# Kernel tuning notes

Measured on AMD Instinct MI355X. Metric: run time of the kernel, lower is better.

The kernel has to match this reference:

```python
import jax, jax.numpy as jnp
import numpy as np

B, T, D, H = 8, 512, 1024, 16
DH = D // H  # per-head feature dim (64)


def setup_inputs() -> dict:
    key = jax.random.key(0)
    ks = jax.random.split(key, 10)
    s = 1.0 / np.sqrt(DH)
    inp = {
        "X_data": jax.random.normal(ks[0], (B, T, D), dtype=jnp.float32),
        "mask": jnp.ones((B, T), dtype=jnp.int32),
        # per-head Q/K/V projections (each SelfAttention has its own d_h x d_h weights)
        "Wq": jax.random.normal(ks[1], (H, DH, DH), dtype=jnp.float32) * s,
        "bq": jnp.zeros((H, DH), dtype=jnp.float32),
        "Wk": jax.random.normal(ks[2], (H, DH, DH), dtype=jnp.float32) * s,
        "bk": jnp.zeros((H, DH), dtype=jnp.float32),
        "Wv": jax.random.normal(ks[3], (H, DH, DH), dtype=jnp.float32) * s,
        "bv": jnp.zeros((H, DH), dtype=jnp.float32),
        # AttentionFusion: linear on concatenated head outputs -> len_feature_new
        "Wf": jax.random.normal(ks[4], (D, D), dtype=jnp.float32) * (1.0 / np.sqrt(D)),
        "bf": jnp.zeros((D,), dtype=jnp.float32),
    }
    return inp


def reference(X_data, mask, Wq, bq, Wk, bk, Wv, bv, Wf, bf):
    # Split features into heads: [B, T, H, DH] (equal partitions since D % H == 0)
    Xh = X_data.reshape(B, T, H, DH)
    # Batched per-head projections (replaces the Python loop over heads)
    Q = jnp.einsum("bthd,hde->bhte", Xh, Wq) + bq[None, :, None, :]
    K = jnp.einsum("bthd,hde->bhte", Xh, Wk) + bk[None, :, None, :]
    V = jnp.einsum("bthd,hde->bhte", Xh, Wv) + bv[None, :, None, :]
    scale = 1.0 / jnp.sqrt(jnp.asarray(DH, dtype=Q.dtype))
    scores = jnp.einsum("bhqe,bhke->bhqk", Q, K) * scale  # [B, H, T, T]
    scores = jnp.where(mask[:, None, None, :] > 0, scores, jnp.asarray(-1e9, scores.dtype))
    att = jax.nn.softmax(scores, axis=-1)
    out = jnp.einsum("bhqk,bhke->bhqe", att, V)  # [B, H, T, DH]
    # Concatenate heads (same order as the per-head loop) and fuse
    out = out.transpose(0, 2, 1, 3).reshape(B, T, D)
    fused = out @ Wf + bf  # AttentionFusion linear
    return fused
```

## Files before the change

kernel.cpp:

```cpp
#include <hip/hip_runtime.h>
#include <math.h>

#define B 8
#define T 512
#define D 1024
#define H 16
#define DH 64

typedef __bf16 bf16;
typedef __attribute__((ext_vector_type(8))) __bf16 bf16x8;
typedef __attribute__((ext_vector_type(4))) __bf16 bf16x4;
typedef __attribute__((ext_vector_type(4))) float f32x4;

__device__ __forceinline__ void gld16(const void* g, void* l) {
    __builtin_amdgcn_global_load_lds(
        (const __attribute__((address_space(1))) void*)g,
        (__attribute__((address_space(3))) void*)l, 16, 0, 0);
}


#define EXP2SCALE 1.44269504088896f

__global__ __launch_bounds__(256, 2) void qkv_attn(
    const float* __restrict__ X, const int* __restrict__ mask,
    const float* __restrict__ Wq, const float* __restrict__ Wk,
    const float* __restrict__ Wv,
    const float* __restrict__ bq, const float* __restrict__ bv,
    const float* __restrict__ Wf, bf16* __restrict__ WfT,
    bf16* __restrict__ Ob)
{
    __shared__ __align__(16) char smem[80384];

    if (blockIdx.x >= 512) {
        bf16* Ts = (bf16*)smem;
        const int ti = blockIdx.x - 512, tid = threadIdx.x;
        const int k0 = (ti >> 4) * 64, n0 = (ti & 15) * 64;
        for (int i = tid; i < 1024; i += 256) {
            const int k = i >> 4, nq = (i & 15) * 4;
            const float4 w = *(const float4*)(Wf + (size_t)(k0 + k) * D + n0 + nq);
            Ts[(nq + 0) * 72 + k] = (bf16)w.x; Ts[(nq + 1) * 72 + k] = (bf16)w.y;
            Ts[(nq + 2) * 72 + k] = (bf16)w.z; Ts[(nq + 3) * 72 + k] = (bf16)w.w;
        }
        __syncthreads();
        for (int i = tid; i < 512; i += 256) {
            const int n = i >> 3, kc = (i & 7) * 8;
            *(bf16x8*)(WfT + (size_t)(n0 + n) * D + k0 + kc) = *(const bf16x8*)&Ts[n * 72 + kc];
        }
        return;
    }

    bf16* Wks = (bf16*)(smem);
    bf16* Wvs = (bf16*)(smem + 8192);
    bf16* Pl  = (bf16*)(smem + 53248);
    bf16* Xkt = (bf16*)(smem + 71680);
    int*  msk = (int*)(smem + 79872);
    bf16* Wqs   = (bf16*)(smem + 16384);
    bf16* Xq    = Pl;
    bf16* Stage = Pl;
    bf16* Ostage = Pl;

    const int bh = blockIdx.x & 127, q0 = (blockIdx.x >> 7) * 128;
    const int b = bh >> 4, h = bh & 15;
    const int tid = threadIdx.x, wave = tid >> 6, lane = tid & 63;
    const int quad = lane >> 4, l15 = lane & 15;

    const int pkrow = wave * 16 + (lane >> 2);
    const int pc0 = (lane & 3) * 2;

    float bqr[4], bvr[4];
#pragma unroll
    for (int nt = 0; nt < 4; ++nt) {
        bqr[nt] = bq[h * DH + nt * 16 + l15];
        bvr[nt] = bv[h * DH + nt * 16 + l15];
    }

    float4 px0, px1, px2, px3;
    {
        const float* src = X + (size_t)(b * T + pkrow) * D + h * DH + pc0 * 8;
        px0 = *(const float4*)src; px1 = *(const float4*)(src + 4);
        px2 = *(const float4*)(src + 8); px3 = *(const float4*)(src + 12);
    }
    int mreg = (tid < 64) ? mask[(size_t)b * T + tid] : 0;

    for (int i = tid; i < 1024; i += 256) {
        const int d = i >> 4, eq4 = (i & 15) * 4;
        const float4 wq4 = *(const float4*)(Wq + (size_t)h * 4096 + d * 64 + eq4);
        const float4 wk4 = *(const float4*)(Wk + (size_t)h * 4096 + d * 64 + eq4);
        const float4 wv4 = *(const float4*)(Wv + (size_t)h * 4096 + d * 64 + eq4);
#pragma unroll
        for (int j = 0; j < 4; ++j) {
            const int e = eq4 + j;
            const int idx = e * 64 + (((d >> 3) ^ (e & 7)) * 8) + (d & 7);
            Wqs[idx] = (bf16)((const float*)&wq4)[j];
            Wks[idx] = (bf16)((const float*)&wk4)[j];
            Wvs[idx] = (bf16)((const float*)&wv4)[j];
        }
    }
    for (int i = tid; i < 1024; i += 256) {
        const int row = i >> 3, c = i & 7;
        const float* src = X + (size_t)(b * T + q0 + row) * D + h * DH + c * 8;
        const float4 x0 = *(const float4*)src;
        const float4 x1 = *(const float4*)(src + 4);
        bf16x8 t;
        t[0] = (bf16)x0.x; t[1] = (bf16)x0.y; t[2] = (bf16)x0.z; t[3] = (bf16)x0.w;
        t[4] = (bf16)x1.x; t[5] = (bf16)x1.y; t[6] = (bf16)x1.z; t[7] = (bf16)x1.w;
        *(bf16x8*)&Xq[row * 64 + ((c ^ (row & 7)) * 8)] = t;
    }
    __syncthreads();

    {
        f32x4 accQ[2][4] = {};
#pragma unroll
        for (int ks = 0; ks < 2; ++ks) {
            bf16x8 af[2], bfr[4];
#pragma unroll
            for (int mt = 0; mt < 2; ++mt) {
                const int row = wave * 32 + mt * 16 + l15;
                af[mt] = *(const bf16x8*)&Xq[row * 64 + (((ks * 4 + quad) ^ (l15 & 7)) * 8)];
            }
#pragma unroll
            for (int nt = 0; nt < 4; ++nt)
                bfr[nt] = *(const bf16x8*)&Wqs[(nt * 16 + l15) * 64 + (((ks * 4 + quad) ^ (l15 & 7)) * 8)];
#pragma unroll
            for (int mt = 0; mt < 2; ++mt)
#pragma unroll
                for (int nt = 0; nt < 4; ++nt)
                    accQ[mt][nt] = __builtin_amdgcn_mfma_f32_16x16x32_bf16(af[mt], bfr[nt], accQ[mt][nt], 0, 0, 0);
        }
        __syncthreads();
        const float qs = 0.125f * EXP2SCALE;
#pragma unroll
        for (int mt = 0; mt < 2; ++mt)
#pragma unroll
            for (int nt = 0; nt < 4; ++nt)
#pragma unroll
                for (int reg = 0; reg < 4; ++reg)
                    Stage[(wave * 32 + mt * 16 + quad * 4 + reg) * 72 + nt * 16 + l15] =
                        (bf16)((accQ[mt][nt][reg] + bqr[nt]) * qs);
        __builtin_amdgcn_wave_barrier();
    }
    bf16x8 qf[2][2];
#pragma unroll
    for (int mt = 0; mt < 2; ++mt)
#pragma unroll
        for (int ks = 0; ks < 2; ++ks)
            qf[mt][ks] = *(const bf16x8*)&Stage[(wave * 32 + mt * 16 + l15) * 72 + ks * 32 + quad * 8];

    f32x4 acc[2][4] = {};
    float lst2[2] = {0.f, 0.f};

    for (int kt = 0; kt < 8; ++kt) {
        const int p = kt & 1;
        bf16* Ks  = (bf16*)(smem + 16384 + p * 9216);
        bf16* Vts = (bf16*)(smem + 34816 + p * 9216);

        {
            bf16x8 t0, t1;
            t0[0] = (bf16)px0.x; t0[1] = (bf16)px0.y; t0[2] = (bf16)px0.z; t0[3] = (bf16)px0.w;
            t0[4] = (bf16)px1.x; t0[5] = (bf16)px1.y; t0[6] = (bf16)px1.z; t0[7] = (bf16)px1.w;
            t1[0] = (bf16)px2.x; t1[1] = (bf16)px2.y; t1[2] = (bf16)px2.z; t1[3] = (bf16)px2.w;
            t1[4] = (bf16)px3.x; t1[5] = (bf16)px3.y; t1[6] = (bf16)px3.z; t1[7] = (bf16)px3.w;
            *(bf16x8*)&Xkt[pkrow * 64 + ((pc0 ^ (pkrow & 7)) * 8)] = t0;
            *(bf16x8*)&Xkt[pkrow * 64 + (((pc0 + 1) ^ (pkrow & 7)) * 8)] = t1;
            if (tid < 64) msk[p * 64 + tid] = mreg;
        }
        __builtin_amdgcn_wave_barrier();

        if (kt < 7) {
            const float* src = X + (size_t)(b * T + (kt + 1) * 64 + pkrow) * D + h * DH + pc0 * 8;
            px0 = *(const float4*)src; px1 = *(const float4*)(src + 4);
            px2 = *(const float4*)(src + 8); px3 = *(const float4*)(src + 12);
            if (tid < 64) mreg = mask[(size_t)b * T + (kt + 1) * 64 + tid];
        }

        {
            bf16x8 afkv[2];
#pragma unroll
            for (int ks = 0; ks < 2; ++ks)
                afkv[ks] = *(const bf16x8*)&Xkt[(wave * 16 + l15) * 64 + (((ks * 4 + quad) ^ (l15 & 7)) * 8)];
            f32x4 accK[4] = {}, accV[4] = {};
            __builtin_amdgcn_s_setprio(1);
#pragma unroll
            for (int ks = 0; ks < 2; ++ks)
#pragma unroll
                for (int nt = 0; nt < 4; ++nt) {
                    const bf16x8 bk8 = *(const bf16x8*)&Wks[(nt * 16 + l15) * 64 + (((ks * 4 + quad) ^ (l15 & 7)) * 8)];
                    accK[nt] = __builtin_amdgcn_mfma_f32_16x16x32_bf16(bk8, afkv[ks], accK[nt], 0, 0, 0);
                    const bf16x8 bv8 = *(const bf16x8*)&Wvs[(nt * 16 + l15) * 64 + (((ks * 4 + quad) ^ (l15 & 7)) * 8)];
                    accV[nt] = __builtin_amdgcn_mfma_f32_16x16x32_bf16(afkv[ks], bv8, accV[nt], 0, 0, 0);
                }
            __builtin_amdgcn_s_setprio(0);
#pragma unroll
            for (int nt = 0; nt < 4; ++nt) {
                bf16x4 kp;
#pragma unroll
                for (int reg = 0; reg < 4; ++reg) kp[reg] = (bf16)accK[nt][reg];
                *(bf16x4*)&Ks[(wave * 16 + l15) * 72 + nt * 16 + quad * 4] = kp;
                bf16x4 vp;
#pragma unroll
                for (int reg = 0; reg < 4; ++reg) vp[reg] = (bf16)accV[nt][reg];
                *(bf16x4*)&Vts[(nt * 16 + l15) * 72 + wave * 16 + quad * 4] = vp;
            }
        }
        asm volatile("s_waitcnt lgkmcnt(0)" ::: "memory");
        __builtin_amdgcn_s_barrier();

        bf16* Plw = Pl + wave * (32 * 72);
        {
            bf16x8 kf[4][2];
#pragma unroll
            for (int nt = 0; nt < 4; ++nt)
#pragma unroll
                for (int ks = 0; ks < 2; ++ks)
                    kf[nt][ks] = *(const bf16x8*)&Ks[(nt * 16 + l15) * 72 + ks * 32 + quad * 8];
            int4 mv4[4];
#pragma unroll
            for (int nt = 0; nt < 4; ++nt)
                mv4[nt] = *(const int4*)&msk[p * 64 + nt * 16 + quad * 4];
#pragma unroll
            for (int mt = 0; mt < 2; ++mt) {
                f32x4 s[4] = {};
                __builtin_amdgcn_s_setprio(1);
#pragma unroll
                for (int ks = 0; ks < 2; ++ks)
#pragma unroll
                    for (int nt = 0; nt < 4; ++nt)
                        s[nt] = __builtin_amdgcn_mfma_f32_16x16x32_bf16(kf[nt][ks], qf[mt][ks], s[nt], 0, 0, 0);
                __builtin_amdgcn_s_setprio(0);
#pragma unroll
                for (int nt = 0; nt < 4; ++nt) {
                    bf16x4 pp;
                    const float p0 = (mv4[nt].x > 0) ? exp2f(s[nt][0]) : 0.f;
                    const float p1 = (mv4[nt].y > 0) ? exp2f(s[nt][1]) : 0.f;
                    const float p2 = (mv4[nt].z > 0) ? exp2f(s[nt][2]) : 0.f;
                    const float p3 = (mv4[nt].w > 0) ? exp2f(s[nt][3]) : 0.f;
                    lst2[mt] += (p0 + p1) + (p2 + p3);
                    pp[0] = (bf16)p0; pp[1] = (bf16)p1; pp[2] = (bf16)p2; pp[3] = (bf16)p3;
                    *(bf16x4*)&Plw[(mt * 16 + l15) * 72 + nt * 16 + quad * 4] = pp;
                }
            }
        }
        __builtin_amdgcn_wave_barrier();

        __builtin_amdgcn_s_setprio(1);
#pragma unroll
        for (int kc = 0; kc < 2; ++kc) {
            const bf16x8 pf0 = *(const bf16x8*)&Plw[(l15) * 72 + kc * 32 + quad * 8];
            const bf16x8 pf1 = *(const bf16x8*)&Plw[(16 + l15) * 72 + kc * 32 + quad * 8];
#pragma unroll
            for (int nt = 0; nt < 4; ++nt) {
                const bf16x8 vf = *(const bf16x8*)&Vts[(nt * 16 + l15) * 72 + kc * 32 + quad * 8];
                acc[0][nt] = __builtin_amdgcn_mfma_f32_16x16x32_bf16(pf0, vf, acc[0][nt], 0, 0, 0);
                acc[1][nt] = __builtin_amdgcn_mfma_f32_16x16x32_bf16(pf1, vf, acc[1][nt], 0, 0, 0);
            }
        }
        __builtin_amdgcn_s_setprio(0);
    }

    __builtin_amdgcn_wave_barrier();
    float inv_r[2][4];
#pragma unroll
    for (int mt = 0; mt < 2; ++mt) {
        float l = lst2[mt];
        l += __shfl_xor(l, 16);
        l += __shfl_xor(l, 32);
        const float inv = 1.f / l;
#pragma unroll
        for (int reg = 0; reg < 4; ++reg)
            inv_r[mt][reg] = __shfl(inv, (lane & 48) | (quad * 4 + reg));
    }
#pragma unroll
    for (int mt = 0; mt < 2; ++mt)
#pragma unroll
        for (int reg = 0; reg < 4; ++reg) {
            const int row = wave * 32 + mt * 16 + quad * 4 + reg;
#pragma unroll
            for (int nt = 0; nt < 4; ++nt)
                Ostage[row * 72 + nt * 16 + l15] =
                    (bf16)(acc[mt][nt][reg] * inv_r[mt][reg] + bvr[nt]);
        }
    __syncthreads();
    for (int i = tid; i < 1024; i += 256) {
        const int row = i >> 3, c = (i & 7) * 8;
        *(bf16x8*)(Ob + ((size_t)b * T + q0 + row) * D + h * DH + c) =
            *(const bf16x8*)&Ostage[row * 72 + c];
    }
}

__global__ __launch_bounds__(512, 4) void fuse_mfma(
    const bf16* __restrict__ Ob, const bf16* __restrict__ WfT,
    const float* __restrict__ bfv, float* __restrict__ out)
{
    __shared__ __align__(16) char smem[73728];

    const int col0 = blockIdx.x * 64;
    const int row0 = blockIdx.y * 128;
    const int tid = threadIdx.x, wave = tid >> 6, lane = tid & 63;
    const int quad = lane >> 4, l15 = lane & 15;
    const int lr = lane >> 3, lc = lane & 7;
    const int wm = (wave >> 1) * 32, wn = (wave & 1) * 32;

    f32x4 acc[2][2] = {};

    auto stage = [&](int t) {
        const int buf = t - (t / 3) * 3;
        bf16* As = (bf16*)(smem + buf * 24576);
        bf16* Bs = (bf16*)(smem + buf * 24576 + 16384);
        const int k0 = t * 64;
#pragma unroll
        for (int j = 0; j < 2; ++j) {
            const int row = wave * 16 + j * 8 + lr;
            gld16(Ob + (size_t)(row0 + row) * D + k0 + ((lc ^ (row & 7)) * 8),
                  &As[(wave * 16 + j * 8) * 64]);
        }
        const int rowB = wave * 8 + lr;
        gld16(WfT + (size_t)(col0 + rowB) * D + k0 + ((lc ^ (rowB & 7)) * 8),
              &Bs[(wave * 8) * 64]);
    };

    stage(0);
    stage(1);

    for (int i = 0; i < 16; ++i) {
        if (i < 15) asm volatile("s_waitcnt vmcnt(3)" ::: "memory");
        else        asm volatile("s_waitcnt vmcnt(0)" ::: "memory");
        __builtin_amdgcn_s_barrier();

        const int buf = i - (i / 3) * 3;
        bf16* As = (bf16*)(smem + buf * 24576);
        bf16* Bs = (bf16*)(smem + buf * 24576 + 16384);
#pragma unroll
        for (int ks = 0; ks < 2; ++ks) {
            bf16x8 af[2], bfr[2];
#pragma unroll
            for (int mt = 0; mt < 2; ++mt)
                af[mt] = *(const bf16x8*)&As[(wm + mt * 16 + l15) * 64 + (((ks * 4 + quad) ^ (l15 & 7)) * 8)];
#pragma unroll
            for (int nt = 0; nt < 2; ++nt)
                bfr[nt] = *(const bf16x8*)&Bs[(wn + nt * 16 + l15) * 64 + (((ks * 4 + quad) ^ (l15 & 7)) * 8)];
#pragma unroll
            for (int mt = 0; mt < 2; ++mt)
#pragma unroll
                for (int nt = 0; nt < 2; ++nt)
                    acc[mt][nt] = __builtin_amdgcn_mfma_f32_16x16x32_bf16(af[mt], bfr[nt], acc[mt][nt], 0, 0, 0);
        }
        if (i < 14) stage(i + 2);
    }
    __syncthreads();

    float* Ofs = (float*)smem;
    float bias[2];
#pragma unroll
    for (int nt = 0; nt < 2; ++nt) bias[nt] = bfv[col0 + wn + nt * 16 + l15];
#pragma unroll
    for (int mt = 0; mt < 2; ++mt)
#pragma unroll
        for (int reg = 0; reg < 4; ++reg) {
            const int row = wm + mt * 16 + quad * 4 + reg;
#pragma unroll
            for (int nt = 0; nt < 2; ++nt)
                Ofs[row * 68 + wn + nt * 16 + l15] = acc[mt][nt][reg] + bias[nt];
        }
    __syncthreads();
    for (int i = tid; i < 2048; i += 512) {
        const int row = i >> 4, c = (i & 15) * 4;
        *(float4*)(out + (size_t)(row0 + row) * D + col0 + c) = *(const float4*)&Ofs[row * 68 + c];
    }
}

extern "C" void kernel_launch(void* const* d_in, const int* in_sizes, int n_in,
                              void* d_out, int out_size, void* d_ws, size_t ws_size,
                              hipStream_t stream) {
    const float* X   = (const float*)d_in[0];
    const int* mask  = (const int*)d_in[1];
    const float* Wq  = (const float*)d_in[2];
    const float* bq  = (const float*)d_in[3];
    const float* Wk  = (const float*)d_in[4];
    const float* bk  = (const float*)d_in[5];
    const float* Wv  = (const float*)d_in[6];
    const float* bv  = (const float*)d_in[7];
    const float* Wf  = (const float*)d_in[8];
    const float* bfv = (const float*)d_in[9];
    float* out = (float*)d_out;
    (void)bk;

    bf16* wsb = (bf16*)d_ws;
    const size_t QN = (size_t)B * H * T * DH;
    bf16* Ob  = wsb;
    bf16* WfT = wsb + QN;

    qkv_attn<<<dim3(768), 256, 0, stream>>>(X, mask, Wq, Wk, Wv, bq, bv, Wf, WfT, Ob);
    fuse_mfma<<<dim3(D / 64, (B * T) / 128), 512, 0, stream>>>(Ob, WfT, bfv, out);
}
```

Before: 123.4 us.

## Fold K projection into Q via Q·Wkᵀ, scoring directly against raw X

Instead of projecting every key tile through Wk, the kernel precomputes Q' = Q·Wkᵀ once per block and computes scores as Q'·Xᵀ against the bf16 X tile. This drops the per-tile K-projection MFMAs, the K staging stores, and the Ks LDS buffer, which shrinks shared memory use. The cost is an extra bf16 rounding of Q' before scoring. The trick relies on bk being zero; a nonzero key bias is no longer applied, although it only adds a per-row constant that softmax cancels.

```diff
diff --git a/kernel.cpp b/kernel.cpp
--- a/kernel.cpp
+++ b/kernel.cpp
@@ -29,7 +29,7 @@
     const float* __restrict__ Wf, bf16* __restrict__ WfT,
     bf16* __restrict__ Ob)
 {
-    __shared__ __align__(16) char smem[80384];
+    __shared__ __align__(16) char smem[61952];
 
     if (blockIdx.x >= 512) {
         bf16* Ts = (bf16*)smem;
@@ -49,13 +49,12 @@
         return;
     }
 
-    bf16* Wks = (bf16*)(smem);
-    bf16* Wvs = (bf16*)(smem + 8192);
-    bf16* Pl  = (bf16*)(smem + 53248);
-    bf16* Xkt = (bf16*)(smem + 71680);
-    int*  msk = (int*)(smem + 79872);
-    bf16* Wqs   = (bf16*)(smem + 16384);
-    bf16* Xq    = Pl;
+    bf16* Wvs  = (bf16*)(smem);
+    bf16* Pl   = (bf16*)(smem + 43008);
+    int*  msk  = (int*)(smem + 61440);
+    bf16* Wqs  = (bf16*)(smem + 8192);
+    bf16* WksT = (bf16*)(smem + 24576);
+    bf16* Xq   = Pl;
     bf16* Stage = Pl;
     bf16* Ostage = Pl;
 
@@ -92,9 +91,12 @@
             const int e = eq4 + j;
             const int idx = e * 64 + (((d >> 3) ^ (e & 7)) * 8) + (d & 7);
             Wqs[idx] = (bf16)((const float*)&wq4)[j];
-            Wks[idx] = (bf16)((const float*)&wk4)[j];
             Wvs[idx] = (bf16)((const float*)&wv4)[j];
         }
+        bf16x4 wkp;
+        wkp[0] = (bf16)wk4.x; wkp[1] = (bf16)wk4.y;
+        wkp[2] = (bf16)wk4.z; wkp[3] = (bf16)wk4.w;
+        *(bf16x4*)&WksT[d * 64 + (((eq4 >> 3) ^ (d & 7)) * 8) + (eq4 & 7)] = wkp;
     }
     for (int i = tid; i < 1024; i += 256) {
         const int row = i >> 3, c = i & 7;
@@ -146,13 +148,44 @@
         for (int ks = 0; ks < 2; ++ks)
             qf[mt][ks] = *(const bf16x8*)&Stage[(wave * 32 + mt * 16 + l15) * 72 + ks * 32 + quad * 8];
 
+    bf16x8 qmf[2][2];
+    {
+        f32x4 accM[2][4] = {};
+#pragma unroll
+        for (int ks = 0; ks < 2; ++ks)
+#pragma unroll
+            for (int nt = 0; nt < 4; ++nt) {
+                const bf16x8 wk8 = *(const bf16x8*)&WksT[(nt * 16 + l15) * 64 + (((ks * 4 + quad) ^ (l15 & 7)) * 8)];
+#pragma unroll
+                for (int mt = 0; mt < 2; ++mt)
+                    accM[mt][nt] = __builtin_amdgcn_mfma_f32_16x16x32_bf16(wk8, qf[mt][ks], accM[mt][nt], 0, 0, 0);
+            }
+        __builtin_amdgcn_wave_barrier();
+#pragma unroll
+        for (int mt = 0; mt < 2; ++mt)
+#pragma unroll
+            for (int nt = 0; nt < 4; ++nt) {
+                bf16x4 qp;
+#pragma unroll
+                for (int reg = 0; reg < 4; ++reg) qp[reg] = (bf16)accM[mt][nt][reg];
+                *(bf16x4*)&Stage[(wave * 32 + mt * 16 + l15) * 72 + nt * 16 + quad * 4] = qp;
+            }
+        __builtin_amdgcn_wave_barrier();
+#pragma unroll
+        for (int mt = 0; mt < 2; ++mt)
+#pragma unroll
+            for (int ks = 0; ks < 2; ++ks)
+                qmf[mt][ks] = *(const bf16x8*)&Stage[(wave * 32 + mt * 16 + l15) * 72 + ks * 32 + quad * 8];
+    }
+    __syncthreads();
+
     f32x4 acc[2][4] = {};
     float lst2[2] = {0.f, 0.f};
 
     for (int kt = 0; kt < 8; ++kt) {
         const int p = kt & 1;
-        bf16* Ks  = (bf16*)(smem + 16384 + p * 9216);
-        bf16* Vts = (bf16*)(smem + 34816 + p * 9216);
+        bf16* Xkt = (bf16*)(smem + 8192 + p * 8192);
+        bf16* Vts = (bf16*)(smem + 24576 + p * 9216);
 
         {
             bf16x8 t0, t1;
@@ -178,24 +211,18 @@
 #pragma unroll
             for (int ks = 0; ks < 2; ++ks)
                 afkv[ks] = *(const bf16x8*)&Xkt[(wave * 16 + l15) * 64 + (((ks * 4 + quad) ^ (l15 & 7)) * 8)];
-            f32x4 accK[4] = {}, accV[4] = {};
+            f32x4 accV[4] = {};
             __builtin_amdgcn_s_setprio(1);
 #pragma unroll
             for (int ks = 0; ks < 2; ++ks)
 #pragma unroll
                 for (int nt = 0; nt < 4; ++nt) {
-                    const bf16x8 bk8 = *(const bf16x8*)&Wks[(nt * 16 + l15) * 64 + (((ks * 4 + quad) ^ (l15 & 7)) * 8)];
-                    accK[nt] = __builtin_amdgcn_mfma_f32_16x16x32_bf16(bk8, afkv[ks], accK[nt], 0, 0, 0);
                     const bf16x8 bv8 = *(const bf16x8*)&Wvs[(nt * 16 + l15) * 64 + (((ks * 4 + quad) ^ (l15 & 7)) * 8)];
                     accV[nt] = __builtin_amdgcn_mfma_f32_16x16x32_bf16(afkv[ks], bv8, accV[nt], 0, 0, 0);
                 }
             __builtin_amdgcn_s_setprio(0);
 #pragma unroll
             for (int nt = 0; nt < 4; ++nt) {
-                bf16x4 kp;
-#pragma unroll
-                for (int reg = 0; reg < 4; ++reg) kp[reg] = (bf16)accK[nt][reg];
-                *(bf16x4*)&Ks[(wave * 16 + l15) * 72 + nt * 16 + quad * 4] = kp;
                 bf16x4 vp;
 #pragma unroll
                 for (int reg = 0; reg < 4; ++reg) vp[reg] = (bf16)accV[nt][reg];
@@ -207,12 +234,12 @@
 
         bf16* Plw = Pl + wave * (32 * 72);
         {
-            bf16x8 kf[4][2];
+            bf16x8 xkf[4][2];
 #pragma unroll
             for (int nt = 0; nt < 4; ++nt)
 #pragma unroll
                 for (int ks = 0; ks < 2; ++ks)
-                    kf[nt][ks] = *(const bf16x8*)&Ks[(nt * 16 + l15) * 72 + ks * 32 + quad * 8];
+                    xkf[nt][ks] = *(const bf16x8*)&Xkt[(nt * 16 + l15) * 64 + (((ks * 4 + quad) ^ (l15 & 7)) * 8)];
             int4 mv4[4];
 #pragma unroll
             for (int nt = 0; nt < 4; ++nt)
@@ -225,7 +252,7 @@
                 for (int ks = 0; ks < 2; ++ks)
 #pragma unroll
                     for (int nt = 0; nt < 4; ++nt)
-                        s[nt] = __builtin_amdgcn_mfma_f32_16x16x32_bf16(kf[nt][ks], qf[mt][ks], s[nt], 0, 0, 0);
+                        s[nt] = __builtin_amdgcn_mfma_f32_16x16x32_bf16(xkf[nt][ks], qmf[mt][ks], s[nt], 0, 0, 0);
                 __builtin_amdgcn_s_setprio(0);
 #pragma unroll
                 for (int nt = 0; nt < 4; ++nt) {
```

Measured after the change: 122.3 us (median of 2 runs). About the same (-0.9%).
